# Performance work log

Hardware: AMD Instinct MI355X
Metric: run time of the kernel (lower is better)

The kernel has to match this reference:

```python
import jax, jax.numpy as jnp
import numpy as np

EPS_COS = 1e-16   # epsilon added to operands (as in the torch module)
EPS_NRM = 1e-8    # torch cosine_similarity clamps norms at 1e-8


def setup_inputs() -> dict:
    key = jax.random.key(0)
    k0, k1, k2, k3, k4, k5 = jax.random.split(key, 6)
    B, N, M = 64, 2048, 256
    stdev = 1.0 / np.sqrt(N + M)
    memory = jax.random.uniform(k0, (B, N, M), jnp.float32, -stdev, stdev)
    k = jax.random.normal(k1, (B, M), jnp.float32)
    g = jax.random.uniform(k2, (B, 1), jnp.float32)
    gamma = jax.random.uniform(k3, (1,), jnp.float32)
    # w_prev[:,0] = w_u_prev, w_prev[:,1] = w_r_prev (positive weightings)
    w_prev = jax.random.uniform(k4, (B, 2, N), jnp.float32)
    # w_lu_prev is a 0/1 least-recently-used mask
    w_lu_prev = jax.random.randint(k5, (B, N), 0, 2, jnp.int32)
    return {"memory": memory, "k": k, "g": g, "gamma": gamma,
            "w_prev": w_prev, "w_lu_prev": w_lu_prev, "n": 4}


def reference(memory, k, g, gamma, w_prev, w_lu_prev, n):
    # --- _similarity: softmax over cosine similarity along memory slots ---
    mem_e = memory + EPS_COS                      # [B, N, M]
    k_e = k[:, None, :] + EPS_COS                 # [B, 1, M]
    num = jnp.einsum('bnm,bom->bn', mem_e, k_e)   # [B, N]
    mem_nrm = jnp.maximum(jnp.linalg.norm(mem_e, axis=-1), EPS_NRM)
    k_nrm = jnp.maximum(jnp.linalg.norm(k_e, axis=-1), EPS_NRM)  # [B, 1]
    w_r = jax.nn.softmax(num / (mem_nrm * k_nrm), axis=-1)       # [B, N]

    # --- interpolate write weighting and usage weighting ---
    w_u_prev = w_prev[:, 0]                        # [B, N]
    w_r_prev = w_prev[:, 1]                        # [B, N]
    w_lu_prev_f = w_lu_prev.astype(memory.dtype)   # [B, N], 0/1 mask
    w_w = g * w_r_prev + (1.0 - g) * w_lu_prev_f   # [B, N]
    w_u = gamma * w_u_prev + w_r + w_w             # [B, N]

    # --- least-used mask: w_u <= n-th smallest usage (per batch) ---
    nth_smallest = jnp.sort(w_u, axis=1)[:, n - 1]           # [B]
    w_lu = (w_u <= nth_smallest[:, None]).astype(memory.dtype)  # [B, N]

    # --- zero out slots that were least-recently-used last step ---
    mem_zeroed = memory * (1.0 - w_lu_prev_f)[..., None]      # [B, N, M]

    # --- lrua_write: rank-1 outer-product write, then read with w_r ---
    mem_new = mem_zeroed + w_w[..., None] * k[:, None, :]     # [B, N, M]
    read = jnp.einsum('bn,bnm->bm', w_r, mem_new)             # [B, M]
    return read
```

## Files before the change

kernel.cpp:

```cpp
#include <hip/hip_runtime.h>
#include <math.h>

#define EPS_COS 1e-16f
#define EPS_NRM 1e-8f

constexpr int B = 64;
constexpr int N = 2048;
constexpr int M = 256;

constexpr int BLK    = 256;
constexpr int WAVES  = BLK / 64;
constexpr int CHUNK  = 128;
constexpr int RPW    = CHUNK / WAVES;
constexpr int PAIRS  = RPW / 2;
constexpr int NCHUNK = N / CHUNK;

__global__ __launch_bounds__(BLK)
void k1_fused(const float* __restrict__ mem,
              const float* __restrict__ kk,
              const float* __restrict__ g,
              const float* __restrict__ w_prev,
              const int*   __restrict__ lu_prev,
              float* __restrict__ pread,
              float* __restrict__ pZ,
              float* __restrict__ pS1)
{
    const int b    = blockIdx.y;
    const int c    = blockIdx.x;
    const int tid  = threadIdx.x;
    const int w    = tid >> 6;
    const int lane = tid & 63;
    const int half = lane >> 5;
    const int sub  = lane & 31;

    float4 ka = *reinterpret_cast<const float4*>(kk + (size_t)b * M + sub * 4);
    float4 kb = *reinterpret_cast<const float4*>(kk + (size_t)b * M + 128 + sub * 4);
    ka.x += EPS_COS; ka.y += EPS_COS; ka.z += EPS_COS; ka.w += EPS_COS;
    kb.x += EPS_COS; kb.y += EPS_COS; kb.z += EPS_COS; kb.w += EPS_COS;
    float ksq = ka.x*ka.x + ka.y*ka.y + ka.z*ka.z + ka.w*ka.w
              + kb.x*kb.x + kb.y*kb.y + kb.z*kb.z + kb.w*kb.w;
#pragma unroll
    for (int off = 16; off; off >>= 1) ksq += __shfl_xor(ksq, off);
    const float kn = fmaxf(sqrtf(ksq), EPS_NRM);

    const float gb   = g[b];
    const float* wrp = w_prev + (size_t)b * 2 * N + N;
    const int*   lup = lu_prev + (size_t)b * N;

    const int rowbase = c * CHUNK + w * RPW;
    const float* p = mem + ((size_t)b * N + rowbase + half) * M + sub * 4;

    float4 accA = make_float4(0.f, 0.f, 0.f, 0.f);
    float4 accB = make_float4(0.f, 0.f, 0.f, 0.f);
    float Zp = 0.f, s1p = 0.f;

    auto process = [&](int i, const float4& va, const float4& vb) {
        float a0 = va.x + EPS_COS, a1 = va.y + EPS_COS;
        float a2 = va.z + EPS_COS, a3 = va.w + EPS_COS;
        float b0 = vb.x + EPS_COS, b1 = vb.y + EPS_COS;
        float b2 = vb.z + EPS_COS, b3 = vb.w + EPS_COS;
        float dot = a0*ka.x + a1*ka.y + a2*ka.z + a3*ka.w
                  + b0*kb.x + b1*kb.y + b2*kb.z + b3*kb.w;
        float msq = a0*a0 + a1*a1 + a2*a2 + a3*a3
                  + b0*b0 + b1*b1 + b2*b2 + b3*b3;
#pragma unroll
        for (int off = 16; off; off >>= 1) {
            dot += __shfl_xor(dot, off);
            msq += __shfl_xor(msq, off);
        }
        const int n = rowbase + 2 * i + half;
        const float cosv = dot / (fmaxf(sqrtf(msq), EPS_NRM) * kn);
        const float e  = __expf(cosv);
        const float lu = (float)lup[n];
        const float ww = gb * wrp[n] + (1.f - gb) * lu;
        Zp += e;
        s1p = fmaf(e, ww, s1p);
        const float cw = e * (1.f - lu);
        accA.x = fmaf(cw, va.x, accA.x);
        accA.y = fmaf(cw, va.y, accA.y);
        accA.z = fmaf(cw, va.z, accA.z);
        accA.w = fmaf(cw, va.w, accA.w);
        accB.x = fmaf(cw, vb.x, accB.x);
        accB.y = fmaf(cw, vb.y, accB.y);
        accB.z = fmaf(cw, vb.z, accB.z);
        accB.w = fmaf(cw, vb.w, accB.w);
    };

    float4 va0 = *reinterpret_cast<const float4*>(p);
    float4 vb0 = *reinterpret_cast<const float4*>(p + 128);
    float4 va1 = *reinterpret_cast<const float4*>(p + 2 * M);
    float4 vb1 = *reinterpret_cast<const float4*>(p + 2 * M + 128);
#pragma unroll 2
    for (int i = 0; i < PAIRS - 2; ++i) {
        float4 va2 = *reinterpret_cast<const float4*>(p + (size_t)(i + 2) * 2 * M);
        float4 vb2 = *reinterpret_cast<const float4*>(p + (size_t)(i + 2) * 2 * M + 128);
        process(i, va0, vb0);
        va0 = va1; vb0 = vb1;
        va1 = va2; vb1 = vb2;
    }
    process(PAIRS - 2, va0, vb0);
    process(PAIRS - 1, va1, vb1);

    accA.x += __shfl_xor(accA.x, 32); accA.y += __shfl_xor(accA.y, 32);
    accA.z += __shfl_xor(accA.z, 32); accA.w += __shfl_xor(accA.w, 32);
    accB.x += __shfl_xor(accB.x, 32); accB.y += __shfl_xor(accB.y, 32);
    accB.z += __shfl_xor(accB.z, 32); accB.w += __shfl_xor(accB.w, 32);
    Zp  += __shfl_xor(Zp, 32);
    s1p += __shfl_xor(s1p, 32);

    __shared__ float sred[WAVES * M];
    __shared__ float sZ[WAVES], sS1[WAVES];
    if (half == 0) {
        *reinterpret_cast<float4*>(&sred[w * M + sub * 4])       = accA;
        *reinterpret_cast<float4*>(&sred[w * M + 128 + sub * 4]) = accB;
    }
    if (lane == 0) { sZ[w] = Zp; sS1[w] = s1p; }
    __syncthreads();

    if (tid < M) {
        float r = 0.f;
#pragma unroll
        for (int q = 0; q < WAVES; ++q) r += sred[q * M + tid];
        pread[((size_t)b * NCHUNK + c) * M + tid] = r;
    }
    if (tid == 0) {
        float z = 0.f, s = 0.f;
#pragma unroll
        for (int q = 0; q < WAVES; ++q) { z += sZ[q]; s += sS1[q]; }
        pZ[b * NCHUNK + c]  = z;
        pS1[b * NCHUNK + c] = s;
    }
}

__global__ __launch_bounds__(M)
void k2_final(const float* __restrict__ pread,
              const float* __restrict__ pZ,
              const float* __restrict__ pS1,
              const float* __restrict__ kk,
              float* __restrict__ out)
{
    const int b = blockIdx.x;
    const int t = threadIdx.x;

    __shared__ float sZ, sS1;
    if (t < 64) {
        float z = (t < NCHUNK) ? pZ[b * NCHUNK + t]  : 0.f;
        float s = (t < NCHUNK) ? pS1[b * NCHUNK + t] : 0.f;
#pragma unroll
        for (int off = 32; off; off >>= 1) {
            z += __shfl_xor(z, off);
            s += __shfl_xor(s, off);
        }
        if (t == 0) { sZ = z; sS1 = s; }
    }
    __syncthreads();

    const float invZ = 1.f / sZ;
    const float* pr = pread + (size_t)b * NCHUNK * M + t;
    float sum = 0.f;
#pragma unroll
    for (int c2 = 0; c2 < NCHUNK; ++c2) sum += pr[(size_t)c2 * M];

    out[(size_t)b * M + t] = (sum + sS1 * kk[(size_t)b * M + t]) * invZ;
}

extern "C" void kernel_launch(void* const* d_in, const int* in_sizes, int n_in,
                              void* d_out, int out_size, void* d_ws, size_t ws_size,
                              hipStream_t stream) {
    const float* mem     = (const float*)d_in[0];
    const float* kk      = (const float*)d_in[1];
    const float* g       = (const float*)d_in[2];
    const float* w_prev  = (const float*)d_in[4];
    const int*   lu_prev = (const int*)  d_in[5];
    float* out = (float*)d_out;

    float* pread = (float*)d_ws;
    float* pZ    = pread + (size_t)B * NCHUNK * M;
    float* pS1   = pZ + (size_t)B * NCHUNK;

    dim3 g1(NCHUNK, B);
    k1_fused<<<g1, BLK, 0, stream>>>(mem, kk, g, w_prev, lu_prev, pread, pZ, pS1);
    k2_final<<<B, M, 0, stream>>>(pread, pZ, pS1, kk, out);
}
```

Baseline: 29.42 us.

## Fuse partial and final reductions into one cooperative kernel with grid sync

Turns the two-kernel pipeline into a single cooperative launch: each block computes its chunk partials, the grid synchronizes, then one block per batch finishes the reduction. Blocks grow to 512 threads with 256-row chunks, which halves the number of partials. The goal is to drop the second launch and its gap. It depends on all 512 blocks being co-resident, and a grid-wide barrier can cost more than the launch it replaces. If the cooperative launch fails, it falls back to the two-kernel path.

```diff
diff --git a/kernel.cpp b/kernel.cpp
--- a/kernel.cpp
+++ b/kernel.cpp
@@ -1,5 +1,8 @@
 #include <hip/hip_runtime.h>
+#include <hip/hip_cooperative_groups.h>
 #include <math.h>
+
+namespace cg = cooperative_groups;
 
 #define EPS_COS 1e-16f
 #define EPS_NRM 1e-8f
@@ -8,25 +11,24 @@
 constexpr int N = 2048;
 constexpr int M = 256;
 
-constexpr int BLK    = 256;
+constexpr int BLK    = 512;
 constexpr int WAVES  = BLK / 64;
-constexpr int CHUNK  = 128;
+constexpr int CHUNK  = 256;
 constexpr int RPW    = CHUNK / WAVES;
 constexpr int PAIRS  = RPW / 2;
 constexpr int NCHUNK = N / CHUNK;
 
-__global__ __launch_bounds__(BLK)
-void k1_fused(const float* __restrict__ mem,
-              const float* __restrict__ kk,
-              const float* __restrict__ g,
-              const float* __restrict__ w_prev,
-              const int*   __restrict__ lu_prev,
-              float* __restrict__ pread,
-              float* __restrict__ pZ,
-              float* __restrict__ pS1)
-{
-    const int b    = blockIdx.y;
-    const int c    = blockIdx.x;
+__device__ __forceinline__
+void phase1(const float* __restrict__ mem,
+            const float* __restrict__ kk,
+            const float* __restrict__ g,
+            const float* __restrict__ w_prev,
+            const int*   __restrict__ lu_prev,
+            float* __restrict__ pread,
+            float* __restrict__ pZ,
+            float* __restrict__ pS1,
+            int b, int c)
+{
     const int tid  = threadIdx.x;
     const int w    = tid >> 6;
     const int lane = tid & 63;
@@ -132,6 +134,53 @@
     }
 }
 
+__global__ __launch_bounds__(BLK, 4)
+void k_coop(const float* __restrict__ mem,
+            const float* __restrict__ kk,
+            const float* __restrict__ g,
+            const float* __restrict__ w_prev,
+            const int*   __restrict__ lu_prev,
+            float* __restrict__ pread,
+            float* __restrict__ pZ,
+            float* __restrict__ pS1,
+            float* __restrict__ out)
+{
+    const int b = blockIdx.y;
+    const int c = blockIdx.x;
+
+    phase1(mem, kk, g, w_prev, lu_prev, pread, pZ, pS1, b, c);
+
+    cg::this_grid().sync();
+
+    if (c == 0 && threadIdx.x < M) {
+        const int t = threadIdx.x;
+        float z = 0.f, s = 0.f;
+#pragma unroll
+        for (int q = 0; q < NCHUNK; ++q) {
+            z += pZ[b * NCHUNK + q];
+            s += pS1[b * NCHUNK + q];
+        }
+        const float* pr = pread + (size_t)b * NCHUNK * M + t;
+        float sum = 0.f;
+#pragma unroll
+        for (int q = 0; q < NCHUNK; ++q) sum += pr[(size_t)q * M];
+        out[(size_t)b * M + t] = (sum + s * kk[(size_t)b * M + t]) / z;
+    }
+}
+
+__global__ __launch_bounds__(BLK, 4)
+void k1_fused(const float* __restrict__ mem,
+              const float* __restrict__ kk,
+              const float* __restrict__ g,
+              const float* __restrict__ w_prev,
+              const int*   __restrict__ lu_prev,
+              float* __restrict__ pread,
+              float* __restrict__ pZ,
+              float* __restrict__ pS1)
+{
+    phase1(mem, kk, g, w_prev, lu_prev, pread, pZ, pS1, blockIdx.y, blockIdx.x);
+}
+
 __global__ __launch_bounds__(M)
 void k2_final(const float* __restrict__ pread,
               const float* __restrict__ pZ,
@@ -141,27 +190,17 @@
 {
     const int b = blockIdx.x;
     const int t = threadIdx.x;
-
-    __shared__ float sZ, sS1;
-    if (t < 64) {
-        float z = (t < NCHUNK) ? pZ[b * NCHUNK + t]  : 0.f;
-        float s = (t < NCHUNK) ? pS1[b * NCHUNK + t] : 0.f;
-#pragma unroll
-        for (int off = 32; off; off >>= 1) {
-            z += __shfl_xor(z, off);
-            s += __shfl_xor(s, off);
-        }
-        if (t == 0) { sZ = z; sS1 = s; }
-    }
-    __syncthreads();
-
-    const float invZ = 1.f / sZ;
+    float z = 0.f, s = 0.f;
+#pragma unroll
+    for (int q = 0; q < NCHUNK; ++q) {
+        z += pZ[b * NCHUNK + q];
+        s += pS1[b * NCHUNK + q];
+    }
     const float* pr = pread + (size_t)b * NCHUNK * M + t;
     float sum = 0.f;
 #pragma unroll
-    for (int c2 = 0; c2 < NCHUNK; ++c2) sum += pr[(size_t)c2 * M];
-
-    out[(size_t)b * M + t] = (sum + sS1 * kk[(size_t)b * M + t]) * invZ;
+    for (int q = 0; q < NCHUNK; ++q) sum += pr[(size_t)q * M];
+    out[(size_t)b * M + t] = (sum + s * kk[(size_t)b * M + t]) / z;
 }
 
 extern "C" void kernel_launch(void* const* d_in, const int* in_sizes, int n_in,
@@ -178,7 +217,16 @@
     float* pZ    = pread + (size_t)B * NCHUNK * M;
     float* pS1   = pZ + (size_t)B * NCHUNK;
 
-    dim3 g1(NCHUNK, B);
-    k1_fused<<<g1, BLK, 0, stream>>>(mem, kk, g, w_prev, lu_prev, pread, pZ, pS1);
-    k2_final<<<B, M, 0, stream>>>(pread, pZ, pS1, kk, out);
-}
+    void* args[] = { (void*)&mem, (void*)&kk, (void*)&g, (void*)&w_prev,
+                     (void*)&lu_prev, (void*)&pread, (void*)&pZ, (void*)&pS1,
+                     (void*)&out };
+    hipError_t err = hipLaunchCooperativeKernel(
+        reinterpret_cast<void*>(k_coop), dim3(NCHUNK, B), dim3(BLK),
+        args, 0, stream);
+
+    if (err != hipSuccess) {
+        dim3 g1(NCHUNK, B);
+        k1_fused<<<g1, BLK, 0, stream>>>(mem, kk, g, w_prev, lu_prev, pread, pZ, pS1);
+        k2_final<<<B, M, 0, stream>>>(pread, pZ, pS1, kk, out);
+    }
+}
```

After: 100.7 us. +242.2%, slower.

## Halve chunk size, preload per-row weights via shuffles, deepen prefetch

Applied to the files above, without the earlier changes.

Halves the rows per block so twice as many blocks cover the memory tensor, and sets an occupancy hint in launch bounds. The per-row mask and write weights are loaded once per wave and broadcast with lane shuffles, which removes scattered scalar loads from the inner loop. The software prefetch is deepened to three row pairs and fully unrolled. The final kernel drops its shared-memory reduction, and every thread now sums the per-chunk partials itself, at the cost of twice as many partials to combine.

```diff
diff --git a/kernel.cpp b/kernel.cpp
--- a/kernel.cpp
+++ b/kernel.cpp
@@ -10,12 +10,12 @@
 
 constexpr int BLK    = 256;
 constexpr int WAVES  = BLK / 64;
-constexpr int CHUNK  = 128;
+constexpr int CHUNK  = 64;
 constexpr int RPW    = CHUNK / WAVES;
 constexpr int PAIRS  = RPW / 2;
 constexpr int NCHUNK = N / CHUNK;
 
-__global__ __launch_bounds__(BLK)
+__global__ __launch_bounds__(BLK, 8)
 void k1_fused(const float* __restrict__ mem,
               const float* __restrict__ kk,
               const float* __restrict__ g,
@@ -33,6 +33,17 @@
     const int half = lane >> 5;
     const int sub  = lane & 31;
 
+    const int rowbase = c * CHUNK + w * RPW;
+
+    const float gb = g[b];
+    float luPre = 0.f, wwPre = 0.f;
+    if (lane < RPW) {
+        const int n = rowbase + lane;
+        const float lu = (float)lu_prev[(size_t)b * N + n];
+        luPre = lu;
+        wwPre = gb * w_prev[(size_t)b * 2 * N + N + n] + (1.f - gb) * lu;
+    }
+
     float4 ka = *reinterpret_cast<const float4*>(kk + (size_t)b * M + sub * 4);
     float4 kb = *reinterpret_cast<const float4*>(kk + (size_t)b * M + 128 + sub * 4);
     ka.x += EPS_COS; ka.y += EPS_COS; ka.z += EPS_COS; ka.w += EPS_COS;
@@ -43,11 +54,6 @@
     for (int off = 16; off; off >>= 1) ksq += __shfl_xor(ksq, off);
     const float kn = fmaxf(sqrtf(ksq), EPS_NRM);
 
-    const float gb   = g[b];
-    const float* wrp = w_prev + (size_t)b * 2 * N + N;
-    const int*   lup = lu_prev + (size_t)b * N;
-
-    const int rowbase = c * CHUNK + w * RPW;
     const float* p = mem + ((size_t)b * N + rowbase + half) * M + sub * 4;
 
     float4 accA = make_float4(0.f, 0.f, 0.f, 0.f);
@@ -68,11 +74,10 @@
             dot += __shfl_xor(dot, off);
             msq += __shfl_xor(msq, off);
         }
-        const int n = rowbase + 2 * i + half;
         const float cosv = dot / (fmaxf(sqrtf(msq), EPS_NRM) * kn);
         const float e  = __expf(cosv);
-        const float lu = (float)lup[n];
-        const float ww = gb * wrp[n] + (1.f - gb) * lu;
+        const float lu = __shfl(luPre, 2 * i + half);
+        const float ww = __shfl(wwPre, 2 * i + half);
         Zp += e;
         s1p = fmaf(e, ww, s1p);
         const float cw = e * (1.f - lu);
@@ -86,20 +91,24 @@
         accB.w = fmaf(cw, vb.w, accB.w);
     };
 
-    float4 va0 = *reinterpret_cast<const float4*>(p);
-    float4 vb0 = *reinterpret_cast<const float4*>(p + 128);
-    float4 va1 = *reinterpret_cast<const float4*>(p + 2 * M);
-    float4 vb1 = *reinterpret_cast<const float4*>(p + 2 * M + 128);
-#pragma unroll 2
-    for (int i = 0; i < PAIRS - 2; ++i) {
-        float4 va2 = *reinterpret_cast<const float4*>(p + (size_t)(i + 2) * 2 * M);
-        float4 vb2 = *reinterpret_cast<const float4*>(p + (size_t)(i + 2) * 2 * M + 128);
-        process(i, va0, vb0);
-        va0 = va1; vb0 = vb1;
-        va1 = va2; vb1 = vb2;
+    float4 a0 = *reinterpret_cast<const float4*>(p);
+    float4 b0 = *reinterpret_cast<const float4*>(p + 128);
+    float4 a1 = *reinterpret_cast<const float4*>(p + 2 * M);
+    float4 b1 = *reinterpret_cast<const float4*>(p + 2 * M + 128);
+    float4 a2 = *reinterpret_cast<const float4*>(p + 4 * M);
+    float4 b2 = *reinterpret_cast<const float4*>(p + 4 * M + 128);
+#pragma unroll
+    for (int i = 0; i < PAIRS - 3; ++i) {
+        float4 a3 = *reinterpret_cast<const float4*>(p + (size_t)(i + 3) * 2 * M);
+        float4 b3 = *reinterpret_cast<const float4*>(p + (size_t)(i + 3) * 2 * M + 128);
+        process(i, a0, b0);
+        a0 = a1; b0 = b1;
+        a1 = a2; b1 = b2;
+        a2 = a3; b2 = b3;
     }
-    process(PAIRS - 2, va0, vb0);
-    process(PAIRS - 1, va1, vb1);
+    process(PAIRS - 3, a0, b0);
+    process(PAIRS - 2, a1, b1);
+    process(PAIRS - 1, a2, b2);
 
     accA.x += __shfl_xor(accA.x, 32); accA.y += __shfl_xor(accA.y, 32);
     accA.z += __shfl_xor(accA.z, 32); accA.w += __shfl_xor(accA.w, 32);
@@ -141,27 +150,17 @@
 {
     const int b = blockIdx.x;
     const int t = threadIdx.x;
-
-    __shared__ float sZ, sS1;
-    if (t < 64) {
-        float z = (t < NCHUNK) ? pZ[b * NCHUNK + t]  : 0.f;
-        float s = (t < NCHUNK) ? pS1[b * NCHUNK + t] : 0.f;
+    float z = 0.f, s = 0.f;
 #pragma unroll
-        for (int off = 32; off; off >>= 1) {
-            z += __shfl_xor(z, off);
-            s += __shfl_xor(s, off);
-        }
-        if (t == 0) { sZ = z; sS1 = s; }
+    for (int q = 0; q < NCHUNK; ++q) {
+        z += pZ[b * NCHUNK + q];
+        s += pS1[b * NCHUNK + q];
     }
-    __syncthreads();
-
-    const float invZ = 1.f / sZ;
     const float* pr = pread + (size_t)b * NCHUNK * M + t;
     float sum = 0.f;
 #pragma unroll
-    for (int c2 = 0; c2 < NCHUNK; ++c2) sum += pr[(size_t)c2 * M];
-
-    out[(size_t)b * M + t] = (sum + sS1 * kk[(size_t)b * M + t]) * invZ;
+    for (int q = 0; q < NCHUNK; ++q) sum += pr[(size_t)q * M];
+    out[(size_t)b * M + t] = (sum + s * kk[(size_t)b * M + t]) / z;
 }
 
 extern "C" void kernel_launch(void* const* d_in, const int* in_sizes, int n_in,
```

Measured after the change: 42.04 us. 42.9% more time.
